# Kernel tuning notes

Measured on AMD Instinct MI355X. Metric: run time of the kernel, lower is better.

Reference implementation:

```python
import jax, jax.numpy as jnp
import numpy as np

DROP_P = 0.5
DROP_KEY = jax.random.key(42)  # fixed key: deterministic dropout mask


def setup_inputs() -> dict:
    key = jax.random.key(0)
    k1, k2, k3 = jax.random.split(key, 3)
    B, H, S, D = 2, 16, 2048, 128
    x1 = jax.random.normal(k1, (B, H, S, D), dtype=jnp.float32)
    x2 = jax.random.normal(k2, (B, H, S, D), dtype=jnp.float32)
    # broadcastable per-head divisor; offset to keep it away from zero
    x3 = jax.random.uniform(k3, (B, H, 1, 1), dtype=jnp.float32) + 1.0
    return {"x1": x1, "x2": x2, "x3": x3}


def reference(x1, x2, x3):
    # v1 = x1 @ x2^T  -> [B,H,S,S]; v2 = v1 / x3 (broadcast divisor)
    scores = jnp.einsum('bhqd,bhkd->bhqk', x1, x2) / x3
    # v3 = softmax over last dim
    probs = jax.nn.softmax(scores, axis=-1)
    # v4 = dropout(p=0.5), training=True semantics: mask and rescale by 1/(1-p)
    keep = jax.random.bernoulli(DROP_KEY, 1.0 - DROP_P, probs.shape)
    probs = jnp.where(keep, probs / (1.0 - DROP_P), 0.0)
    # v5 = v4 @ x1 (note: values are x1, not a separate V); v6 = v5 + x2 residual
    out = jnp.einsum('bhqk,bhkd->bhqd', probs, x1) + x2
    return out
```

## Files before the change

### kernel.cpp

```cpp
#include <hip/hip_runtime.h>
#include <math.h>


constexpr int Sc = 2048, Dc = 128;
constexpr int NT = 32;
constexpr int BUF = 32768;
constexpr int VREL = 16384;
constexpr int POFF = 65536;

typedef short bf16x8 __attribute__((ext_vector_type(8)));
typedef float f32x4 __attribute__((ext_vector_type(4)));
union U8 { uint4 u; bf16x8 v; };

__device__ __forceinline__ unsigned rotl(unsigned x, int r) {
  return __builtin_amdgcn_alignbit(x, x, 32 - r);
}

__device__ __forceinline__ unsigned tf_o0(unsigned x1) {
  const unsigned ks1 = 42u;
  const unsigned ks2 = 0x1BD11BDAu ^ 42u;
  unsigned x0 = 0u; x1 += ks1;
#define TFR(r) { x0 += x1; x1 = rotl(x1, r); x1 ^= x0; }
  TFR(13) TFR(15) TFR(26) TFR(6)
  x0 += ks1; x1 += ks2 + 1u;
  TFR(17) TFR(29) TFR(16) TFR(24)
  x0 += ks2; x1 += 0u + 2u;
  TFR(13) TFR(15) TFR(26) TFR(6)
  x1 += ks1 + 3u;
  TFR(17) TFR(29) TFR(16) TFR(24)
  x0 += ks1; x1 += ks2 + 4u;
  TFR(13) TFR(15) TFR(26)
  x0 += x1;
  x0 += ks2;
#undef TFR
  return x0;
}

__device__ __forceinline__ unsigned kb(unsigned mw, int pos) {
  return (unsigned)(((int)(mw << (31 - pos))) >> 31);
}

__device__ __forceinline__ unsigned pk2rn(float a, float b) {
  return __builtin_amdgcn_perm(__float_as_uint(b) + 0x8000u,
                               __float_as_uint(a) + 0x8000u, 0x07060302u);
}

__device__ __forceinline__ unsigned hw2(unsigned ma, unsigned mb) {
  return __builtin_amdgcn_perm(mb, ma, 0x05040100u);
}

__device__ __forceinline__ void gload16(const void* g, void* l) {
  __builtin_amdgcn_global_load_lds(
      (const __attribute__((address_space(1))) void*)g,
      (__attribute__((address_space(3))) void*)l, 16, 0, 0);
}

__global__ __launch_bounds__(256)
void prepack(const float* __restrict__ x1, const float* __restrict__ x2,
             uint4* __restrict__ Kb, uint4* __restrict__ Vt,
             unsigned* __restrict__ Mw) {
  __shared__ ushort Kl[32 * 136];
  __shared__ ushort Vl[32 * 136];
  __shared__ ushort Ml[32 * 128];
  const int tid = threadIdx.x;
  const size_t tile = blockIdx.x;
  const float4* ks = (const float4*)(x2 + tile * 4096);
  const float4* vs = (const float4*)(x1 + tile * 4096);
#pragma unroll
  for (int it = 0; it < 4; ++it) {
    int f = it * 256 + tid;
    int row = f >> 5, c4 = f & 31;
    float4 kv = ks[f];
    float4 vv = vs[f];
    *(uint2*)&Kl[row * 136 + c4 * 4] = uint2{pk2rn(kv.x, kv.y), pk2rn(kv.z, kv.w)};
    *(uint2*)&Vl[row * 136 + c4 * 4] = uint2{pk2rn(vv.x, vv.y), pk2rn(vv.z, vv.w)};
  }

  {
    const unsigned a    = (unsigned)tile * 128u + (unsigned)(tid >> 1);
    const unsigned th   = (unsigned)(tid & 1);
    const unsigned ablk = a >> 8, atid = a & 255u;
    const unsigned bh = ablk & 31u, qt = ablk >> 5;
    const unsigned wv = atid >> 6, ln = atid & 63u;
    const unsigned g = ln >> 4, q = ln & 15u;
    const unsigned row = bh * 2048u + qt * 64u + wv * 16u + q;
    const unsigned fb = row * 2048u + g * 4u + th * 1024u;
    const int atid2 = tid >> 1;
    for (int tt = 0; tt < 16; ++tt) {
      unsigned w = 0;
#pragma unroll
      for (int h2 = 0; h2 < 4; ++h2)
#pragma unroll
        for (int i = 0; i < 4; ++i) {
          unsigned o0 = tf_o0(fb + (unsigned)(tt * 64 + h2 * 16 + i));
          w |= (o0 >> 31) << (h2 * 4 + i);
        }
      Ml[(th * 16 + tt) * 128 + atid2] = (ushort)(~w & 0xFFFFu);
    }
  }
  __syncthreads();

#pragma unroll
  for (int it = 0; it < 2; ++it) {
    int u = it * 256 + tid;
    int lane = u & 63, grp = u >> 6;
    int mt = grp >> 2, c = grp & 3, m16 = lane & 15, g = lane >> 4;
    Kb[tile * 512 + u] = *(const uint4*)&Kl[(mt * 16 + m16) * 136 + c * 32 + g * 8];
  }
#pragma unroll
  for (int it = 0; it < 2; ++it) {
    int u = it * 256 + tid;
    int lane = u & 63, dt = u >> 6, m16 = lane & 15, g = lane >> 4;
    int d = dt * 16 + m16, k0 = g * 8;
    unsigned w[4];
#pragma unroll
    for (int p = 0; p < 4; ++p) {
      unsigned lo = Vl[(k0 + 2 * p) * 136 + d];
      unsigned hi = Vl[(k0 + 2 * p + 1) * 136 + d];
      w[p] = lo | (hi << 16);
    }
    Vt[tile * 512 + u] = uint4{w[0], w[1], w[2], w[3]};
  }

  {
    const unsigned ablk = (unsigned)(tile >> 1), h = (unsigned)(tile & 1);
    const unsigned* Mu = (const unsigned*)Ml;
#pragma unroll
    for (int k = 0; k < 8; ++k) {
      int L = tid + k * 256;
      int t = L >> 6, j2 = L & 63;
      Mw[ablk * 4096u + (unsigned)t * 128u + h * 64u + (unsigned)j2] = Mu[L];
    }
  }
}

__global__ __launch_bounds__(256, 2)
void attn8(const uint4* __restrict__ Kb, const uint4* __restrict__ Vt,
           const ushort* __restrict__ Mwu,
           const float* __restrict__ x1, const float* __restrict__ x2,
           const float* __restrict__ x3, float* __restrict__ out) {
  __shared__ uint4 smemv[(POFF + 8192) / 16];
  char* smem = (char*)smemv;
  float* Os = (float*)smem;

  const int tid = threadIdx.x, wave = tid >> 6, lane = tid & 63;
  const int g = lane >> 4, q = lane & 15;
  const int blk = blockIdx.x, bh = blk & 31, qt = blk >> 5;

  const float* X1 = x1 + (size_t)bh * (Sc * Dc);
  const float* X2 = x2 + (size_t)bh * (Sc * Dc);
  float* outp = out + (size_t)bh * (Sc * Dc);
  const float cl2 = (1.0f / x3[bh]) * 1.4426950408889634f;

  const int qrow = qt * 64 + wave * 16 + q;
  char* prow = smem + POFF + wave * 2048 + q * 128;

  const size_t tg = (size_t)bh * 64;
  const int off = wave * 1024 + lane * 16;
  const unsigned mbase = (unsigned)blk * 8192u + (unsigned)tid;

  auto issue = [&](int tt, int bb) {
    const char* kg = (const char*)(Kb + (tg + 2 * tt) * 512);
    const char* vg = (const char*)(Vt + (tg + 2 * tt) * 512);
#pragma unroll
    for (int h = 0; h < 2; ++h) {
      gload16(kg + h * 8192 + off,        smem + bb + h * 8192 + off);
      gload16(kg + h * 8192 + off + 4096, smem + bb + h * 8192 + off + 4096);
      gload16(vg + h * 8192 + off,        smem + bb + VREL + h * 8192 + off);
      gload16(vg + h * 8192 + off + 4096, smem + bb + VREL + h * 8192 + off + 4096);
    }
  };

  bf16x8 qf[4];
  {
    const float4* qsrc = (const float4*)(X1 + (size_t)qrow * Dc);
#pragma unroll
    for (int c = 0; c < 4; ++c) {
      float4 f0 = qsrc[c * 8 + g * 2], f1 = qsrc[c * 8 + g * 2 + 1];
      U8 cv; cv.u = uint4{pk2rn(f0.x, f0.y), pk2rn(f0.z, f0.w),
                          pk2rn(f1.x, f1.y), pk2rn(f1.z, f1.w)};
      qf[c] = cv.v;
    }
  }

  f32x4 o[8];
#pragma unroll
  for (int i = 0; i < 8; ++i) o[i] = f32x4{0.f, 0.f, 0.f, 0.f};
  float l_run = 0.0f;

  issue(0, 0);
  __builtin_amdgcn_sched_barrier(0);
  unsigned mwc = Mwu[mbase];
  unsigned mwn = 0;

  for (int t = 0; t < NT; ++t) {
    __syncthreads();

    if (t < NT - 1) {
      issue(t + 1, ((t + 1) & 1) * BUF);
      mwn = Mwu[mbase + (unsigned)(t + 1) * 256u];
    }
    __builtin_amdgcn_sched_barrier(0);

    const char* kb_ = smem + (t & 1) * BUF;
    const char* vb = kb_ + VREL;

    f32x4 s0 = {}, s1 = {}, s2 = {}, s3 = {};
#pragma unroll
    for (int c = 0; c < 4; ++c) {
      U8 a0; a0.u = *(const uint4*)(kb_ +        ((0 * 4 + c) * 64 + lane) * 16);
      U8 a1; a1.u = *(const uint4*)(kb_ +        ((1 * 4 + c) * 64 + lane) * 16);
      U8 a2; a2.u = *(const uint4*)(kb_ + 8192 + ((0 * 4 + c) * 64 + lane) * 16);
      U8 a3; a3.u = *(const uint4*)(kb_ + 8192 + ((1 * 4 + c) * 64 + lane) * 16);
      s0 = __builtin_amdgcn_mfma_f32_16x16x32_bf16(a0.v, qf[c], s0, 0, 0, 0);
      s1 = __builtin_amdgcn_mfma_f32_16x16x32_bf16(a1.v, qf[c], s1, 0, 0, 0);
      s2 = __builtin_amdgcn_mfma_f32_16x16x32_bf16(a2.v, qf[c], s2, 0, 0, 0);
      s3 = __builtin_amdgcn_mfma_f32_16x16x32_bf16(a3.v, qf[c], s3, 0, 0, 0);
    }

    float pr[16];
    float ls = 0.0f;
#pragma unroll
    for (int i = 0; i < 4; ++i) { pr[i]      = __builtin_amdgcn_exp2f(s0[i] * cl2); ls += pr[i]; }
#pragma unroll
    for (int i = 0; i < 4; ++i) { pr[4 + i]  = __builtin_amdgcn_exp2f(s1[i] * cl2); ls += pr[4 + i]; }
#pragma unroll
    for (int i = 0; i < 4; ++i) { pr[8 + i]  = __builtin_amdgcn_exp2f(s2[i] * cl2); ls += pr[8 + i]; }
#pragma unroll
    for (int i = 0; i < 4; ++i) { pr[12 + i] = __builtin_amdgcn_exp2f(s3[i] * cl2); ls += pr[12 + i]; }
    ls += __shfl_xor(ls, 16);
    ls += __shfl_xor(ls, 32);
    l_run += ls;

#pragma unroll
    for (int h2 = 0; h2 < 4; ++h2) {
      unsigned m0 = hw2(kb(mwc, h2 * 4 + 0), kb(mwc, h2 * 4 + 1));
      unsigned m1 = hw2(kb(mwc, h2 * 4 + 2), kb(mwc, h2 * 4 + 3));
      unsigned w0 = pk2rn(pr[h2 * 4 + 0], pr[h2 * 4 + 1]) & m0;
      unsigned w1 = pk2rn(pr[h2 * 4 + 2], pr[h2 * 4 + 3]) & m1;
      int u = (h2 >> 1) * 8 + (h2 & 1) * 4 + g;
      *(uint2*)(prow + ((u ^ q) & 15) * 8) = uint2{w0, w1};
    }

    U8 bf0, bf1;
    {
      int u0 = 2 * g;
      uint2 lo0 = *(const uint2*)(prow + (((u0 + 0) ^ q) & 15) * 8);
      uint2 hi0 = *(const uint2*)(prow + (((u0 + 1) ^ q) & 15) * 8);
      bf0.u = uint4{lo0.x, lo0.y, hi0.x, hi0.y};
      int u1 = 8 + 2 * g;
      uint2 lo1 = *(const uint2*)(prow + (((u1 + 0) ^ q) & 15) * 8);
      uint2 hi1 = *(const uint2*)(prow + (((u1 + 1) ^ q) & 15) * 8);
      bf1.u = uint4{lo1.x, lo1.y, hi1.x, hi1.y};
    }

#pragma unroll
    for (int dt = 0; dt < 8; ++dt) {
      U8 av0; av0.u = *(const uint4*)(vb +        (dt * 64 + lane) * 16);
      U8 av1; av1.u = *(const uint4*)(vb + 8192 + (dt * 64 + lane) * 16);
      o[dt] = __builtin_amdgcn_mfma_f32_16x16x32_bf16(av0.v, bf0.v, o[dt], 0, 0, 0);
      o[dt] = __builtin_amdgcn_mfma_f32_16x16x32_bf16(av1.v, bf1.v, o[dt], 0, 0, 0);
    }

    mwc = mwn;
  }

  const float invl = 2.0f / l_run;
  __syncthreads();
  {
    float* ow = Os + (size_t)(wave * 16 + q) * 132;
#pragma unroll
    for (int dt = 0; dt < 8; ++dt) {
      int d = dt * 16 + g * 4;
      *(float4*)&ow[d] = float4{o[dt][0] * invl, o[dt][1] * invl,
                                o[dt][2] * invl, o[dt][3] * invl};
    }
  }
  __syncthreads();
#pragma unroll
  for (int it = 0; it < 8; ++it) {
    int f = it * 256 + tid;
    int ql = f >> 5, c4 = f & 31;
    float4 ov = *(const float4*)&Os[ql * 132 + c4 * 4];
    size_t goff = (size_t)(qt * 64 + ql) * Dc + c4 * 4;
    float4 xv = *(const float4*)&X2[goff];
    *(float4*)&outp[goff] = float4{ov.x + xv.x, ov.y + xv.y, ov.z + xv.z, ov.w + xv.w};
  }
}

extern "C" void kernel_launch(void* const* d_in, const int* in_sizes, int n_in,
                              void* d_out, int out_size, void* d_ws, size_t ws_size,
                              hipStream_t stream) {
  const float* x1 = (const float*)d_in[0];
  const float* x2 = (const float*)d_in[1];
  const float* x3 = (const float*)d_in[2];
  float* out = (float*)d_out;
  const size_t PREP = (size_t)2048 * 512 * 16;
  uint4* Kb = (uint4*)d_ws;
  uint4* Vtg = (uint4*)((char*)d_ws + PREP);
  unsigned* Mw = (unsigned*)((char*)d_ws + 2 * PREP);
  prepack<<<2048, 256, 0, stream>>>(x1, x2, Kb, Vtg, Mw);
  attn8<<<1024, 256, 0, stream>>>(Kb, Vtg, (const ushort*)Mw, x1, x2, x3, out);
}
```

Baseline: 410.2 us.

## Split dropout mask generation between prepack and attention kernel

The first TS key tiles now get their dropout masks from Threefry computed inline in the attention kernel, interleaved with the MFMA work. The prepack kernel only generates masks for the remaining tiles. The aim is to shrink the ALU-heavy prepack RNG phase and hide part of that work under the attention kernel's matrix ops. The cost is extra VALU work and registers in the attention loop, which could hurt occupancy or MFMA throughput.

```diff
diff --git a/kernel.cpp b/kernel.cpp
--- a/kernel.cpp
+++ b/kernel.cpp
@@ -4,6 +4,7 @@
 
 constexpr int Sc = 2048, Dc = 128;
 constexpr int NT = 32;
+constexpr int TS = 12;
 constexpr int BUF = 32768;
 constexpr int VREL = 16384;
 constexpr int POFF = 65536;
@@ -36,6 +37,10 @@
   return x0;
 }
 
+__device__ __forceinline__ unsigned keepmask(unsigned idx) {
+  return (unsigned)(((int)~tf_o0(idx)) >> 31);
+}
+
 __device__ __forceinline__ unsigned kb(unsigned mw, int pos) {
   return (unsigned)(((int)(mw << (31 - pos))) >> 31);
 }
@@ -53,6 +58,16 @@
   __builtin_amdgcn_global_load_lds(
       (const __attribute__((address_space(1))) void*)g,
       (__attribute__((address_space(3))) void*)l, 16, 0, 0);
+}
+
+__device__ __forceinline__ void masks8(unsigned ib, unsigned km[8]) {
+#pragma unroll
+  for (int h2 = 0; h2 < 4; ++h2) {
+    unsigned a0 = keepmask(ib + h2 * 16 + 0), a1 = keepmask(ib + h2 * 16 + 1);
+    unsigned a2 = keepmask(ib + h2 * 16 + 2), a3 = keepmask(ib + h2 * 16 + 3);
+    km[h2 * 2 + 0] = hw2(a0, a1);
+    km[h2 * 2 + 1] = hw2(a2, a3);
+  }
 }
 
 __global__ __launch_bounds__(256)
@@ -77,25 +92,28 @@
   }
 
   {
-    const unsigned a    = (unsigned)tile * 128u + (unsigned)(tid >> 1);
-    const unsigned th   = (unsigned)(tid & 1);
+    const unsigned a    = (unsigned)tile * 128u + (unsigned)(tid & 127);
+    const unsigned th   = (unsigned)(tid >> 7);
     const unsigned ablk = a >> 8, atid = a & 255u;
     const unsigned bh = ablk & 31u, qt = ablk >> 5;
     const unsigned wv = atid >> 6, ln = atid & 63u;
     const unsigned g = ln >> 4, q = ln & 15u;
     const unsigned row = bh * 2048u + qt * 64u + wv * 16u + q;
-    const unsigned fb = row * 2048u + g * 4u + th * 1024u;
-    const int atid2 = tid >> 1;
-    for (int tt = 0; tt < 16; ++tt) {
+    const unsigned fb = row * 2048u + g * 4u;
+    const int atid2 = tid & 127;
+    const int half = (NT - TS) >> 1;
+    const int tbeg = TS + (int)th * half;
+    for (int k = 0; k < half; ++k) {
+      int t = tbeg + k;
       unsigned w = 0;
 #pragma unroll
       for (int h2 = 0; h2 < 4; ++h2)
 #pragma unroll
         for (int i = 0; i < 4; ++i) {
-          unsigned o0 = tf_o0(fb + (unsigned)(tt * 64 + h2 * 16 + i));
+          unsigned o0 = tf_o0(fb + (unsigned)(t * 64 + h2 * 16 + i));
           w |= (o0 >> 31) << (h2 * 4 + i);
         }
-      Ml[(th * 16 + tt) * 128 + atid2] = (ushort)(~w & 0xFFFFu);
+      Ml[t * 128 + atid2] = (ushort)(~w & 0xFFFFu);
     }
   }
   __syncthreads();
@@ -135,7 +153,7 @@
 }
 
 __global__ __launch_bounds__(256, 2)
-void attn8(const uint4* __restrict__ Kb, const uint4* __restrict__ Vt,
+void attn9(const uint4* __restrict__ Kb, const uint4* __restrict__ Vt,
            const ushort* __restrict__ Mwu,
            const float* __restrict__ x1, const float* __restrict__ x2,
            const float* __restrict__ x3, float* __restrict__ out) {
@@ -153,6 +171,7 @@
   const float cl2 = (1.0f / x3[bh]) * 1.4426950408889634f;
 
   const int qrow = qt * 64 + wave * 16 + q;
+  const unsigned row_base = (unsigned)(bh * Sc + qrow) * (unsigned)Sc;
   char* prow = smem + POFF + wave * 2048 + q * 128;
 
   const size_t tg = (size_t)bh * 64;
@@ -190,7 +209,8 @@
 
   issue(0, 0);
   __builtin_amdgcn_sched_barrier(0);
-  unsigned mwc = Mwu[mbase];
+  unsigned kmc[8], kmn[8];
+  masks8(row_base + (unsigned)(g * 4), kmc);
   unsigned mwn = 0;
 
   for (int t = 0; t < NT; ++t) {
@@ -198,7 +218,7 @@
 
     if (t < NT - 1) {
       issue(t + 1, ((t + 1) & 1) * BUF);
-      mwn = Mwu[mbase + (unsigned)(t + 1) * 256u];
+      if (t + 1 >= TS) mwn = Mwu[mbase + (unsigned)(t + 1) * 256u];
     }
     __builtin_amdgcn_sched_barrier(0);
 
@@ -218,6 +238,16 @@
       s3 = __builtin_amdgcn_mfma_f32_16x16x32_bf16(a3.v, qf[c], s3, 0, 0, 0);
     }
 
+    if (t + 1 < TS) {
+      masks8(row_base + (unsigned)((t + 1) * 64) + (unsigned)(g * 4), kmn);
+    } else if (t + 1 < NT) {
+#pragma unroll
+      for (int h2 = 0; h2 < 4; ++h2) {
+        kmn[h2 * 2 + 0] = hw2(kb(mwn, h2 * 4 + 0), kb(mwn, h2 * 4 + 1));
+        kmn[h2 * 2 + 1] = hw2(kb(mwn, h2 * 4 + 2), kb(mwn, h2 * 4 + 3));
+      }
+    }
+
     float pr[16];
     float ls = 0.0f;
 #pragma unroll
@@ -234,10 +264,8 @@
 
 #pragma unroll
     for (int h2 = 0; h2 < 4; ++h2) {
-      unsigned m0 = hw2(kb(mwc, h2 * 4 + 0), kb(mwc, h2 * 4 + 1));
-      unsigned m1 = hw2(kb(mwc, h2 * 4 + 2), kb(mwc, h2 * 4 + 3));
-      unsigned w0 = pk2rn(pr[h2 * 4 + 0], pr[h2 * 4 + 1]) & m0;
-      unsigned w1 = pk2rn(pr[h2 * 4 + 2], pr[h2 * 4 + 3]) & m1;
+      unsigned w0 = pk2rn(pr[h2 * 4 + 0], pr[h2 * 4 + 1]) & kmc[h2 * 2 + 0];
+      unsigned w1 = pk2rn(pr[h2 * 4 + 2], pr[h2 * 4 + 3]) & kmc[h2 * 2 + 1];
       int u = (h2 >> 1) * 8 + (h2 & 1) * 4 + g;
       *(uint2*)(prow + ((u ^ q) & 15) * 8) = uint2{w0, w1};
     }
@@ -262,7 +290,8 @@
       o[dt] = __builtin_amdgcn_mfma_f32_16x16x32_bf16(av1.v, bf1.v, o[dt], 0, 0, 0);
     }
 
-    mwc = mwn;
+#pragma unroll
+    for (int i = 0; i < 8; ++i) kmc[i] = kmn[i];
   }
 
   const float invl = 2.0f / l_run;
@@ -300,5 +329,5 @@
   uint4* Vtg = (uint4*)((char*)d_ws + PREP);
   unsigned* Mw = (unsigned*)((char*)d_ws + 2 * PREP);
   prepack<<<2048, 256, 0, stream>>>(x1, x2, Kb, Vtg, Mw);
-  attn8<<<1024, 256, 0, stream>>>(Kb, Vtg, (const ushort*)Mw, x1, x2, x3, out);
-}
+  attn9<<<1024, 256, 0, stream>>>(Kb, Vtg, (const ushort*)Mw, x1, x2, x3, out);
+}
```

Result: no change. 411.2 us (+0.2%).
